# Kernel tuning notes

Hardware: AMD Instinct MI355X
Metric: run time of the kernel (lower is better)

The kernel has to match this reference:

```python
import jax, jax.numpy as jnp
import numpy as np

ITER_STEPS = 2  # matches init_kwargs iteration_steps


def setup_inputs() -> dict:
    key = jax.random.key(0)
    ks = jax.random.split(key, 7)
    B, N, D = 16, 1024, 128
    s = 1.0 / np.sqrt(D).astype(np.float32)
    return {
        "node": jax.random.normal(ks[0], (B, N, D), jnp.float32),
        "node_mask": jax.random.randint(ks[1], (B, N), 0, 2, jnp.int32),
        "graph": jax.random.randint(ks[2], (B, N, N), 0, 2, jnp.int32),
        "w_weight": jax.random.normal(ks[3], (D, 1), jnp.float32) * s,
        "b_weight": jnp.zeros((1,), jnp.float32),
        "w_self": jax.random.normal(ks[4], (D, D), jnp.float32) * s,
        "b_self": jnp.zeros((D,), jnp.float32),
        "w_left": jax.random.normal(ks[5], (D, D), jnp.float32) * s,
        "w_right": jax.random.normal(ks[6], (D, D), jnp.float32) * s,
    }


def reference(node, node_mask, graph, w_weight, b_weight, w_self, b_self, w_left, w_right):
    B, N, D = node.shape
    dt = node.dtype
    nm = node_mask.astype(dt)
    g = graph.astype(dt)  # graph[:, :N, :N] slice is identity here
    diag = jnp.eye(N, dtype=dt)
    # pairwise validity mask, zero diagonal (no self loops)
    pair = nm[:, None, :] * nm[:, :, None] * (1.0 - diag)
    gl = pair * g            # edges present in graph
    gr = pair * (1.0 - g)    # complement edges
    nnum = gl.sum(-1) + gr.sum(-1)
    # replace_masked_values(nnum, nnum>=1, 1): avoid div-by-zero for isolated nodes
    nnum = jnp.where(nnum >= 1.0, nnum, jnp.ones((), dt))
    ws = []
    for _ in range(ITER_STEPS):
        node_weight = jax.nn.sigmoid(node @ w_weight + b_weight)[..., 0]  # [B, N]
        ws.append(node_weight)
        self_info = node @ w_self + b_self
        # replace_masked_values(weight_bcast, mask, 0) == weight * mask (mask is 0/1)
        left = jnp.einsum('bij,bjd->bid', node_weight[:, None, :] * gl, node @ w_left)
        right = jnp.einsum('bij,bjd->bid', node_weight[:, None, :] * gr, node @ w_right)
        node = jax.nn.relu(self_info + (left + right) / nnum[..., None])
    all_node_weight = jnp.stack(ws, axis=1)  # [B, ITER_STEPS, N]
    return node, all_node_weight
```

## Files before the change

kernel.cpp:

```cpp
#include <hip/hip_runtime.h>
#include <math.h>


constexpr int B = 16, N = 1024, D = 128, ITERS = 2;

typedef unsigned short u16;
typedef unsigned char u8;
typedef unsigned int u32;
typedef __attribute__((ext_vector_type(8))) short short8v;
typedef __attribute__((ext_vector_type(4))) unsigned int uint4v;
typedef __attribute__((ext_vector_type(4))) float float4v;

__device__ inline u16 f32_to_bf16(float f) {
  u32 bits = __float_as_uint(f);
  bits += 0x7FFFu + ((bits >> 16) & 1u);
  return (u16)(bits >> 16);
}

__device__ __forceinline__ void map_brt(int blk, int& b, int& rt) {
  int slot = blk >> 3;
  b = ((slot >> 6) << 3) | (blk & 7);
  rt = slot & 63;
}

__global__ __launch_bounds__(256) void wpack_kernel(
    const float* __restrict__ w_self, const float* __restrict__ w_left,
    const float* __restrict__ w_right, const int* __restrict__ mask,
    u16* __restrict__ wsF, u16* __restrict__ wlF, u16* __restrict__ wrF,
    float* __restrict__ sb) {
  int blk = blockIdx.x, tid = threadIdx.x;
  if (blk < 12) {
    int widx = blk >> 2, seg = blk & 3;
    const float* W = (widx == 0) ? w_self : (widx == 1) ? w_left : w_right;
    u16* WF = (widx == 0) ? wsF : (widx == 1) ? wlF : wrF;
#pragma unroll
    for (int q = 0; q < 16; ++q) {
      int o = seg * 4096 + q * 256 + tid;
      int e = o & 7, lane = (o >> 3) & 63, ks = (o >> 9) & 3, cblk = o >> 11;
      int c = cblk * 16 + (lane & 15);
      int k = ks * 32 + ((lane >> 4) & 3) * 8 + e;
      WF[o] = f32_to_bf16(W[k * 128 + c]);
    }
  } else {
    int b = tid >> 4, seg = tid & 15;
    const int* mp = mask + b * N + seg * 64;
    int s = 0;
    for (int q = 0; q < 64; ++q) s += mp[q];
    float fs = (float)s;
    fs += __shfl_xor(fs, 8, 16);
    fs += __shfl_xor(fs, 4, 16);
    fs += __shfl_xor(fs, 2, 16);
    fs += __shfl_xor(fs, 1, 16);
    if (seg == 0) sb[b] = fs;
  }
}

__device__ __forceinline__ void prep_body(
    float (*nlds)[132], float* wmrow, float* invrow, int b, int rt, int tid,
    const int* __restrict__ mask, const float* __restrict__ w_weight,
    const float* __restrict__ b_weight, const float* __restrict__ b_self,
    const u16* __restrict__ wsF, const u16* __restrict__ wlF,
    const u16* __restrict__ wrF, const float* __restrict__ sb,
    float* __restrict__ outw_t, float* __restrict__ nsadj, u16* __restrict__ xF,
    float* __restrict__ part) {
  int r0 = rt * 16;
  if (tid < 128) {
    int r = tid >> 3, jj = tid & 7;
    float acc = 0.f;
#pragma unroll
    for (int q = 0; q < 4; ++q) {
      float4 wv = *(const float4*)(w_weight + jj * 16 + q * 4);
      const float* np = &nlds[r][jj * 16 + q * 4];
      acc += np[0] * wv.x + np[1] * wv.y + np[2] * wv.z + np[3] * wv.w;
    }
    acc += __shfl_xor(acc, 4, 8);
    acc += __shfl_xor(acc, 2, 8);
    acc += __shfl_xor(acc, 1, 8);
    if (jj == 0) {
      float w = 1.f / (1.f + expf(-(acc + b_weight[0])));
      outw_t[b * (ITERS * N) + r0 + r] = w;
      float nm = (float)mask[b * N + r0 + r];
      float nnum = fmaxf(nm * (sb[b] - nm), 1.f);
      wmrow[r] = w * nm;
      invrow[r] = nm / nnum;
    }
  }
  __syncthreads();

  int w = tid >> 6, lane = tid & 63;
  int l15 = lane & 15, lg = lane >> 4;
  int ch = w * 32;

  short8v af[4];
#pragma unroll
  for (int ks = 0; ks < 4; ++ks) {
    float tmp[8];
    *(float4*)&tmp[0] = *(const float4*)&nlds[l15][ks * 32 + lg * 8];
    *(float4*)&tmp[4] = *(const float4*)&nlds[l15][ks * 32 + lg * 8 + 4];
    short8v t;
#pragma unroll
    for (int e = 0; e < 8; ++e) t[e] = (short)f32_to_bf16(tmp[e]);
    af[ks] = t;
  }

  float4v aNR[2], aNL[2], aNS[2];
#define RUN_GEMM(WF, ACC)                                                          \
  {                                                                                \
    _Pragma("unroll") for (int cf = 0; cf < 2; ++cf) {                             \
      ACC[cf] = (float4v){0.f, 0.f, 0.f, 0.f};                                     \
      int cblk = w * 2 + cf;                                                       \
      const u16* bp = (WF) + (((cblk * 4) * 64 + lane) << 3);                      \
      _Pragma("unroll") for (int ks = 0; ks < 4; ++ks) {                           \
        short8v bf = *(const short8v*)(bp + ks * 512);                             \
        ACC[cf] =                                                                  \
            __builtin_amdgcn_mfma_f32_16x16x32_bf16(af[ks], bf, ACC[cf], 0, 0, 0); \
      }                                                                            \
    }                                                                              \
  }
  RUN_GEMM(wrF, aNR);
  RUN_GEMM(wlF, aNL);
  RUN_GEMM(wsF, aNS);
#undef RUN_GEMM

  float wmv[4], invv[4];
#pragma unroll
  for (int j = 0; j < 4; ++j) {
    int rloc = lg * 4 + j;
    wmv[j] = wmrow[rloc];
    invv[j] = invrow[rloc];
  }
  int kch = rt >> 1;
  int lane_f = ((rt & 1) * 2 + (lg >> 1)) * 16;
  int e0 = (lg & 1) * 4;
  float pv[2] = {0.f, 0.f};
#pragma unroll
  for (int cf = 0; cf < 2; ++cf) {
    int col = ch + cf * 16 + l15;
    float bsv = b_self[col];
    u16 xb[4];
#pragma unroll
    for (int j = 0; j < 4; ++j) {
      float x = wmv[j] * (aNL[cf][j] - aNR[cf][j]);
      float v = wmv[j] * aNR[cf][j];
      pv[cf] += v;
      nsadj[((size_t)b * N + r0 + lg * 4 + j) * D + col] =
          aNS[cf][j] + bsv - invv[j] * v;
      xb[j] = f32_to_bf16(x);
    }
    int cblk = w * 2 + cf;
    size_t fi = ((((size_t)b * 8 + cblk) * 32 + kch) * 64 + lane_f + l15) * 8 + e0;
    *(ushort4*)&xF[fi] = *(ushort4*)&xb[0];
  }
#pragma unroll
  for (int cf = 0; cf < 2; ++cf) {
    pv[cf] += __shfl_xor(pv[cf], 16);
    pv[cf] += __shfl_xor(pv[cf], 32);
  }
  if (lg == 0) {
#pragma unroll
    for (int cf = 0; cf < 2; ++cf)
      part[((size_t)b * 64 + rt) * 128 + ch + cf * 16 + l15] = pv[cf];
  }
}

__device__ __forceinline__ void agg_tile(
    const u8* __restrict__ gpk, const u16* __restrict__ xF,
    const float* __restrict__ part, const float* __restrict__ sb,
    const int* __restrict__ mask, const float* __restrict__ nsadj, int b, int r0,
    int tid, float (*accbuf)[16][132], float* vt_s, float ov[8]) {
  if (tid < 128) {
    float s = 0.f;
#pragma unroll
    for (int p = 0; p < 64; ++p) s += part[((size_t)b * 64 + p) * 128 + tid];
    vt_s[tid] = s;
  }
  int w = tid >> 6, lane = tid & 63;
  int l15 = lane & 15, lg = lane >> 4;
  int ks = w;
  const u8* gr = gpk + ((size_t)b * N + r0 + l15) * 128 + lg * 32 + ks * 8;
  uint2 q = *(const uint2*)gr;
  u32 qa[2] = {q.x, q.y};

  const u16* xb = xF + ((((size_t)b * 8) * 32 + ks * 8) * 64 + lane) * 8;

  float4v acc[8] = {{0.f, 0.f, 0.f, 0.f}, {0.f, 0.f, 0.f, 0.f},
                    {0.f, 0.f, 0.f, 0.f}, {0.f, 0.f, 0.f, 0.f},
                    {0.f, 0.f, 0.f, 0.f}, {0.f, 0.f, 0.f, 0.f},
                    {0.f, 0.f, 0.f, 0.f}, {0.f, 0.f, 0.f, 0.f}};
  short8v bcur[8], bnxt[8];
#pragma unroll
  for (int cf = 0; cf < 8; ++cf) bcur[cf] = *(const short8v*)(xb + cf * 16384);
#pragma unroll
  for (int cl = 0; cl < 8; ++cl) {
    if (cl + 1 < 8) {
#pragma unroll
      for (int cf = 0; cf < 8; ++cf)
        bnxt[cf] = *(const short8v*)(xb + cf * 16384 + (cl + 1) * 512);
    }
    u32 by = (qa[cl >> 2] >> ((cl & 3) * 8)) & 255u;
    u32 e0 = ((by & 1u) ? 0x3F80u : 0u) | ((by & 2u) ? 0x3F800000u : 0u);
    u32 e1 = ((by & 4u) ? 0x3F80u : 0u) | ((by & 8u) ? 0x3F800000u : 0u);
    u32 e2 = ((by & 16u) ? 0x3F80u : 0u) | ((by & 32u) ? 0x3F800000u : 0u);
    u32 e3 = ((by & 64u) ? 0x3F80u : 0u) | ((by & 128u) ? 0x3F800000u : 0u);
    uint4v ev = {e0, e1, e2, e3};
    short8v a = __builtin_bit_cast(short8v, ev);
#pragma unroll
    for (int cf = 0; cf < 8; ++cf)
      acc[cf] =
          __builtin_amdgcn_mfma_f32_16x16x32_bf16(a, bcur[cf], acc[cf], 0, 0, 0);
#pragma unroll
    for (int cf = 0; cf < 8; ++cf) bcur[cf] = bnxt[cf];
  }
#pragma unroll
  for (int cf = 0; cf < 8; ++cf)
#pragma unroll
    for (int j = 0; j < 4; ++j) accbuf[w][lg * 4 + j][cf * 16 + l15] = acc[cf][j];
  __syncthreads();

  int row = w * 4 + (lane >> 4);
  int colb = (tid & 15) * 8;
  int orow = r0 + row;
  float nm = (float)mask[b * N + orow];
  float sbv = sb[b];
  float nnum = fmaxf(nm * (sbv - nm), 1.f);
  float inv = nm / nnum;
  const float* nsp = nsadj + ((size_t)b * N + orow) * D + colb;
  float4 n0 = *(const float4*)nsp;
  float4 n1 = *(const float4*)(nsp + 4);
  float nsa[8] = {n0.x, n0.y, n0.z, n0.w, n1.x, n1.y, n1.z, n1.w};
#pragma unroll
  for (int e = 0; e < 8; ++e) {
    int c = colb + e;
    float m = accbuf[0][row][c] + accbuf[1][row][c] + accbuf[2][row][c] +
              accbuf[3][row][c] + vt_s[c];
    ov[e] = fmaxf(nsa[e] + inv * m, 0.f);
  }
}

__global__ __launch_bounds__(256, 4) void pack_prep_kernel(
    const float* __restrict__ node, const int* __restrict__ graph,
    const int* __restrict__ mask, const float* __restrict__ w_weight,
    const float* __restrict__ b_weight, const float* __restrict__ b_self,
    const u16* __restrict__ wsF, const u16* __restrict__ wlF,
    const u16* __restrict__ wrF, const float* __restrict__ sb,
    u8* __restrict__ gpk, float* __restrict__ outw, float* __restrict__ nsadjA,
    u16* __restrict__ xFA, float* __restrict__ partA) {
  __shared__ float nlds[16][132];
  __shared__ float wmrow[16], invrow[16];
  int tid = threadIdx.x;
  int blk = blockIdx.x;

  if (blk < 2048) {
    int gidx = blk * 256 + tid;
#pragma unroll
    for (int it = 0; it < 4; ++it, gidx += 2048 * 256) {
      int j = gidx & 127;
      int rowg = gidx >> 7;
      int i = rowg & (N - 1);
      const int* gp = graph + ((size_t)rowg << 10) + j * 8;
      int4 a = *(const int4*)gp;
      int4 c = *(const int4*)(gp + 4);
      u32 by = (u32)(a.x != 0) | ((u32)(a.y != 0) << 1) | ((u32)(a.z != 0) << 2) |
               ((u32)(a.w != 0) << 3) | ((u32)(c.x != 0) << 4) |
               ((u32)(c.y != 0) << 5) | ((u32)(c.z != 0) << 6) |
               ((u32)(c.w != 0) << 7);
      if (j == (i >> 3)) by &= ~(1u << (i & 7));
      gpk[((size_t)rowg << 7) + (j & 3) * 32 + (j >> 2)] = (u8)by;
    }
    return;
  }

  int pblk = blk - 2048;
  int b, rt;
  map_brt(pblk, b, rt);
  int r0 = rt * 16;

  const float* nbase = node + ((size_t)b * N + r0) * D;
#pragma unroll
  for (int p = 0; p < 2; ++p) {
    int g = p * 256 + tid;
    int row = g >> 5, c4 = g & 31;
    *(float4*)&nlds[row][c4 * 4] = *(const float4*)(nbase + row * 128 + c4 * 4);
  }
  __syncthreads();

  prep_body(nlds, wmrow, invrow, b, rt, tid, mask, w_weight, b_weight, b_self, wsF,
            wlF, wrF, sb, outw, nsadjA, xFA, partA);
}

__global__ __launch_bounds__(256, 3) void agg_prep_kernel(
    const u8* __restrict__ gpk, const int* __restrict__ mask,
    const float* __restrict__ w_weight, const float* __restrict__ b_weight,
    const float* __restrict__ b_self, const u16* __restrict__ wsF,
    const u16* __restrict__ wlF, const u16* __restrict__ wrF,
    const float* __restrict__ sb, const float* __restrict__ nsadjA,
    const u16* __restrict__ xFA, const float* __restrict__ partA,
    float* __restrict__ outw, float* __restrict__ nsadjB, u16* __restrict__ xFB,
    float* __restrict__ partB) {
  __shared__ float accbuf[4][16][132];
  __shared__ float vt_s[128];
  __shared__ float nlds[16][132];
  __shared__ float wmrow[16], invrow[16];
  int tid = threadIdx.x;
  int b, rt;
  map_brt(blockIdx.x, b, rt);
  int r0 = rt * 16;

  float ov[8];
  agg_tile(gpk, xFA, partA, sb, mask, nsadjA, b, r0, tid, accbuf, vt_s, ov);

  int row = (tid >> 6) * 4 + ((tid & 63) >> 4);
  int colb = (tid & 15) * 8;
#pragma unroll
  for (int e = 0; e < 8; ++e) nlds[row][colb + e] = ov[e];
  __syncthreads();

  prep_body(nlds, wmrow, invrow, b, rt, tid, mask, w_weight, b_weight, b_self, wsF,
            wlF, wrF, sb, outw + N , nsadjB, xFB, partB);
}

__global__ __launch_bounds__(256, 4) void agg_fin_kernel(
    const u8* __restrict__ gpk, const int* __restrict__ mask,
    const float* __restrict__ sb, const float* __restrict__ nsadjB,
    const u16* __restrict__ xFB, const float* __restrict__ partB,
    float* __restrict__ out) {
  __shared__ float accbuf[4][16][132];
  __shared__ float vt_s[128];
  int tid = threadIdx.x;
  int b, rt;
  map_brt(blockIdx.x, b, rt);
  int r0 = rt * 16;

  float ov[8];
  agg_tile(gpk, xFB, partB, sb, mask, nsadjB, b, r0, tid, accbuf, vt_s, ov);

  int row = (tid >> 6) * 4 + ((tid & 63) >> 4);
  int colb = (tid & 15) * 8;
  float* op = out + ((size_t)b * N + r0 + row) * D + colb;
  float4 o0 = {ov[0], ov[1], ov[2], ov[3]};
  float4 o1 = {ov[4], ov[5], ov[6], ov[7]};
  *(float4*)op = o0;
  *(float4*)(op + 4) = o1;
}

extern "C" void kernel_launch(void* const* d_in, const int* in_sizes, int n_in,
                              void* d_out, int out_size, void* d_ws, size_t ws_size,
                              hipStream_t stream) {
  const float* node0 = (const float*)d_in[0];
  const int* mask = (const int*)d_in[1];
  const int* graph = (const int*)d_in[2];
  const float* w_weight = (const float*)d_in[3];
  const float* b_weight = (const float*)d_in[4];
  const float* w_self = (const float*)d_in[5];
  const float* b_self = (const float*)d_in[6];
  const float* w_left = (const float*)d_in[7];
  const float* w_right = (const float*)d_in[8];
  float* out = (float*)d_out;
  float* outw = out + (size_t)B * N * D;

  char* ws = (char*)d_ws;
  const size_t MB = 1024 * 1024;
  float* nsadjA = (float*)ws;
  float* nsadjB = (float*)(ws + 8 * MB);
  u16* xFA = (u16*)(ws + 16 * MB);
  u16* xFB = (u16*)(ws + 20 * MB);
  u8* gpk = (u8*)(ws + 24 * MB);
  u16* wsF = (u16*)(ws + 26 * MB);
  u16* wlF = wsF + 16384;
  u16* wrF = wlF + 16384;
  float* partA = (float*)(ws + 26 * MB + 3 * 32768);
  float* partB = partA + (size_t)B * 64 * 128;
  float* sb = partB + (size_t)B * 64 * 128;

  wpack_kernel<<<13, 256, 0, stream>>>(w_self, w_left, w_right, mask, wsF, wlF,
                                       wrF, sb);
  pack_prep_kernel<<<3072, 256, 0, stream>>>(node0, graph, mask, w_weight,
                                             b_weight, b_self, wsF, wlF, wrF, sb,
                                             gpk, outw, nsadjA, xFA, partA);
  agg_prep_kernel<<<1024, 256, 0, stream>>>(gpk, mask, w_weight, b_weight, b_self,
                                            wsF, wlF, wrF, sb, nsadjA, xFA, partA,
                                            outw, nsadjB, xFB, partB);
  agg_fin_kernel<<<1024, 256, 0, stream>>>(gpk, mask, sb, nsadjB, xFB, partB, out);
}
```

Before: 67.44 us.

## Aggregate 32-row tiles with per-wave column split and 512-thread blocks

The aggregation kernels now give each block 32 output rows with 512 threads. Each wave owns a 16-column slice and runs the full K loop over two row sets, so each B fragment is reused for two MFMAs. This removes the cross-wave LDS reduction over K and halves redundant xF reads per row. The part-sum reduction is split across thread groups, and the graph packing loop issues all its loads before processing. The cost is a longer serial MFMA dependency chain per wave and less latency hiding from fewer, larger blocks.

```diff
diff --git a/kernel.cpp b/kernel.cpp
--- a/kernel.cpp
+++ b/kernel.cpp
@@ -15,6 +15,15 @@
   u32 bits = __float_as_uint(f);
   bits += 0x7FFFu + ((bits >> 16) & 1u);
   return (u16)(bits >> 16);
+}
+
+__device__ __forceinline__ short8v expand_byte(u32 by) {
+  u32 e0 = ((by & 1u) ? 0x3F80u : 0u) | ((by & 2u) ? 0x3F800000u : 0u);
+  u32 e1 = ((by & 4u) ? 0x3F80u : 0u) | ((by & 8u) ? 0x3F800000u : 0u);
+  u32 e2 = ((by & 16u) ? 0x3F80u : 0u) | ((by & 32u) ? 0x3F800000u : 0u);
+  u32 e3 = ((by & 64u) ? 0x3F80u : 0u) | ((by & 128u) ? 0x3F800000u : 0u);
+  uint4v ev = {e0, e1, e2, e3};
+  return __builtin_bit_cast(short8v, ev);
 }
 
 __device__ __forceinline__ void map_brt(int blk, int& b, int& rt) {
@@ -163,78 +172,73 @@
   }
 }
 
-__device__ __forceinline__ void agg_tile(
+__device__ __forceinline__ void agg32_core(
     const u8* __restrict__ gpk, const u16* __restrict__ xF,
     const float* __restrict__ part, const float* __restrict__ sb,
     const int* __restrict__ mask, const float* __restrict__ nsadj, int b, int r0,
-    int tid, float (*accbuf)[16][132], float* vt_s, float ov[8]) {
-  if (tid < 128) {
+    int tid, float (*red)[128], float ov[8]) {
+  {
+    int col = tid & 127, grp = tid >> 7;
     float s = 0.f;
 #pragma unroll
-    for (int p = 0; p < 64; ++p) s += part[((size_t)b * 64 + p) * 128 + tid];
-    vt_s[tid] = s;
-  }
-  int w = tid >> 6, lane = tid & 63;
+    for (int p = 0; p < 16; ++p)
+      s += part[((size_t)b * 64 + grp * 16 + p) * 128 + col];
+    red[grp][col] = s;
+  }
+  int wv = tid >> 6, lane = tid & 63;
   int l15 = lane & 15, lg = lane >> 4;
-  int ks = w;
-  const u8* gr = gpk + ((size_t)b * N + r0 + l15) * 128 + lg * 32 + ks * 8;
-  uint2 q = *(const uint2*)gr;
-  u32 qa[2] = {q.x, q.y};
-
-  const u16* xb = xF + ((((size_t)b * 8) * 32 + ks * 8) * 64 + lane) * 8;
-
-  float4v acc[8] = {{0.f, 0.f, 0.f, 0.f}, {0.f, 0.f, 0.f, 0.f},
-                    {0.f, 0.f, 0.f, 0.f}, {0.f, 0.f, 0.f, 0.f},
-                    {0.f, 0.f, 0.f, 0.f}, {0.f, 0.f, 0.f, 0.f},
-                    {0.f, 0.f, 0.f, 0.f}, {0.f, 0.f, 0.f, 0.f}};
-  short8v bcur[8], bnxt[8];
-#pragma unroll
-  for (int cf = 0; cf < 8; ++cf) bcur[cf] = *(const short8v*)(xb + cf * 16384);
-#pragma unroll
-  for (int cl = 0; cl < 8; ++cl) {
-    if (cl + 1 < 8) {
-#pragma unroll
-      for (int cf = 0; cf < 8; ++cf)
-        bnxt[cf] = *(const short8v*)(xb + cf * 16384 + (cl + 1) * 512);
-    }
-    u32 by = (qa[cl >> 2] >> ((cl & 3) * 8)) & 255u;
-    u32 e0 = ((by & 1u) ? 0x3F80u : 0u) | ((by & 2u) ? 0x3F800000u : 0u);
-    u32 e1 = ((by & 4u) ? 0x3F80u : 0u) | ((by & 8u) ? 0x3F800000u : 0u);
-    u32 e2 = ((by & 16u) ? 0x3F80u : 0u) | ((by & 32u) ? 0x3F800000u : 0u);
-    u32 e3 = ((by & 64u) ? 0x3F80u : 0u) | ((by & 128u) ? 0x3F800000u : 0u);
-    uint4v ev = {e0, e1, e2, e3};
-    short8v a = __builtin_bit_cast(short8v, ev);
-#pragma unroll
-    for (int cf = 0; cf < 8; ++cf)
-      acc[cf] =
-          __builtin_amdgcn_mfma_f32_16x16x32_bf16(a, bcur[cf], acc[cf], 0, 0, 0);
-#pragma unroll
-    for (int cf = 0; cf < 8; ++cf) bcur[cf] = bnxt[cf];
-  }
-#pragma unroll
-  for (int cf = 0; cf < 8; ++cf)
-#pragma unroll
-    for (int j = 0; j < 4; ++j) accbuf[w][lg * 4 + j][cf * 16 + l15] = acc[cf][j];
+
+  const u8* g0 = gpk + ((size_t)b * N + r0 + l15) * 128 + lg * 32;
+  uint4 qA = *(const uint4*)g0;
+  uint4 qB = *(const uint4*)(g0 + 16);
+  uint4 qC = *(const uint4*)(g0 + 16 * 128);
+  uint4 qD = *(const uint4*)(g0 + 16 * 128 + 16);
+  u32 q0[8] = {qA.x, qA.y, qA.z, qA.w, qB.x, qB.y, qB.z, qB.w};
+  u32 q1[8] = {qC.x, qC.y, qC.z, qC.w, qD.x, qD.y, qD.z, qD.w};
+
+  const u16* xb = xF + (((size_t)b * 8 + wv) * 32) * 512 + lane * 8;
+
+  float4v acc0 = {0.f, 0.f, 0.f, 0.f};
+  float4v acc1 = {0.f, 0.f, 0.f, 0.f};
+  short8v b0 = *(const short8v*)(xb);
+  short8v b1 = *(const short8v*)(xb + 512);
+#pragma unroll
+  for (int cl = 0; cl < 32; ++cl) {
+    short8v b2 = b0;
+    if (cl + 2 < 32) b2 = *(const short8v*)(xb + (cl + 2) * 512);
+    u32 by0 = (q0[cl >> 2] >> ((cl & 3) * 8)) & 255u;
+    u32 by1 = (q1[cl >> 2] >> ((cl & 3) * 8)) & 255u;
+    short8v a0 = expand_byte(by0);
+    short8v a1 = expand_byte(by1);
+    acc0 = __builtin_amdgcn_mfma_f32_16x16x32_bf16(a0, b0, acc0, 0, 0, 0);
+    acc1 = __builtin_amdgcn_mfma_f32_16x16x32_bf16(a1, b0, acc1, 0, 0, 0);
+    b0 = b1;
+    b1 = b2;
+  }
   __syncthreads();
 
-  int row = w * 4 + (lane >> 4);
-  int colb = (tid & 15) * 8;
-  int orow = r0 + row;
-  float nm = (float)mask[b * N + orow];
   float sbv = sb[b];
-  float nnum = fmaxf(nm * (sbv - nm), 1.f);
-  float inv = nm / nnum;
-  const float* nsp = nsadj + ((size_t)b * N + orow) * D + colb;
-  float4 n0 = *(const float4*)nsp;
-  float4 n1 = *(const float4*)(nsp + 4);
-  float nsa[8] = {n0.x, n0.y, n0.z, n0.w, n1.x, n1.y, n1.z, n1.w};
-#pragma unroll
-  for (int e = 0; e < 8; ++e) {
-    int c = colb + e;
-    float m = accbuf[0][row][c] + accbuf[1][row][c] + accbuf[2][row][c] +
-              accbuf[3][row][c] + vt_s[c];
-    ov[e] = fmaxf(nsa[e] + inv * m, 0.f);
-  }
+  int col = wv * 16 + l15;
+  float vt = red[0][col] + red[1][col] + red[2][col] + red[3][col];
+#pragma unroll
+  for (int rs = 0; rs < 2; ++rs) {
+#pragma unroll
+    for (int j = 0; j < 4; ++j) {
+      float a = (rs == 0) ? acc0[j] : acc1[j];
+      int orow = r0 + rs * 16 + lg * 4 + j;
+      float nm = (float)mask[b * N + orow];
+      float nnum = fmaxf(nm * (sbv - nm), 1.f);
+      float inv = nm / nnum;
+      size_t off = ((size_t)b * N + orow) * D + col;
+      ov[rs * 4 + j] = fmaxf(nsadj[off] + inv * (a + vt), 0.f);
+    }
+  }
+}
+
+__device__ __forceinline__ void map_brt32(int blk, int& b, int& rt32) {
+  int slot = blk >> 3;
+  b = ((slot >> 5) << 3) | (blk & 7);
+  rt32 = slot & 31;
 }
 
 __global__ __launch_bounds__(256, 4) void pack_prep_kernel(
@@ -251,15 +255,22 @@
   int blk = blockIdx.x;
 
   if (blk < 2048) {
-    int gidx = blk * 256 + tid;
-#pragma unroll
-    for (int it = 0; it < 4; ++it, gidx += 2048 * 256) {
-      int j = gidx & 127;
-      int rowg = gidx >> 7;
+    int gidx0 = blk * 256 + tid;
+    int4 ra[4][2];
+#pragma unroll
+    for (int it = 0; it < 4; ++it) {
+      int gidx = gidx0 + it * (2048 * 256);
+      int j = gidx & 127, rowg = gidx >> 7;
+      const int* gp = graph + ((size_t)rowg << 10) + j * 8;
+      ra[it][0] = *(const int4*)gp;
+      ra[it][1] = *(const int4*)(gp + 4);
+    }
+#pragma unroll
+    for (int it = 0; it < 4; ++it) {
+      int gidx = gidx0 + it * (2048 * 256);
+      int j = gidx & 127, rowg = gidx >> 7;
       int i = rowg & (N - 1);
-      const int* gp = graph + ((size_t)rowg << 10) + j * 8;
-      int4 a = *(const int4*)gp;
-      int4 c = *(const int4*)(gp + 4);
+      int4 a = ra[it][0], c = ra[it][1];
       u32 by = (u32)(a.x != 0) | ((u32)(a.y != 0) << 1) | ((u32)(a.z != 0) << 2) |
                ((u32)(a.w != 0) << 3) | ((u32)(c.x != 0) << 4) |
                ((u32)(c.y != 0) << 5) | ((u32)(c.z != 0) << 6) |
@@ -288,7 +299,7 @@
             wlF, wrF, sb, outw, nsadjA, xFA, partA);
 }
 
-__global__ __launch_bounds__(256, 3) void agg_prep_kernel(
+__global__ __launch_bounds__(512, 4) void agg_prep_kernel(
     const u8* __restrict__ gpk, const int* __restrict__ mask,
     const float* __restrict__ w_weight, const float* __restrict__ b_weight,
     const float* __restrict__ b_self, const u16* __restrict__ wsF,
@@ -297,50 +308,57 @@
     const u16* __restrict__ xFA, const float* __restrict__ partA,
     float* __restrict__ outw, float* __restrict__ nsadjB, u16* __restrict__ xFB,
     float* __restrict__ partB) {
-  __shared__ float accbuf[4][16][132];
-  __shared__ float vt_s[128];
-  __shared__ float nlds[16][132];
-  __shared__ float wmrow[16], invrow[16];
+  __shared__ float red[4][128];
+  __shared__ float nlds[32][132];
+  __shared__ float wmrow[32], invrow[32];
   int tid = threadIdx.x;
-  int b, rt;
-  map_brt(blockIdx.x, b, rt);
-  int r0 = rt * 16;
+  int b, rt32;
+  map_brt32(blockIdx.x, b, rt32);
+  int r0 = rt32 * 32;
 
   float ov[8];
-  agg_tile(gpk, xFA, partA, sb, mask, nsadjA, b, r0, tid, accbuf, vt_s, ov);
-
-  int row = (tid >> 6) * 4 + ((tid & 63) >> 4);
-  int colb = (tid & 15) * 8;
-#pragma unroll
-  for (int e = 0; e < 8; ++e) nlds[row][colb + e] = ov[e];
+  agg32_core(gpk, xFA, partA, sb, mask, nsadjA, b, r0, tid, red, ov);
+
+  int wv = tid >> 6, lane = tid & 63;
+  int l15 = lane & 15, lg = lane >> 4;
+  int col = wv * 16 + l15;
+#pragma unroll
+  for (int rs = 0; rs < 2; ++rs)
+#pragma unroll
+    for (int j = 0; j < 4; ++j) nlds[rs * 16 + lg * 4 + j][col] = ov[rs * 4 + j];
   __syncthreads();
 
-  prep_body(nlds, wmrow, invrow, b, rt, tid, mask, w_weight, b_weight, b_self, wsF,
-            wlF, wrF, sb, outw + N , nsadjB, xFB, partB);
-}
-
-__global__ __launch_bounds__(256, 4) void agg_fin_kernel(
+  int half = tid >> 8;
+  int tid2 = tid & 255;
+  prep_body((float(*)[132]) & nlds[half * 16][0], &wmrow[half * 16],
+            &invrow[half * 16], b, rt32 * 2 + half, tid2, mask, w_weight,
+            b_weight, b_self, wsF, wlF, wrF, sb, outw + N, nsadjB, xFB, partB);
+}
+
+__global__ __launch_bounds__(512, 4) void agg_fin_kernel(
     const u8* __restrict__ gpk, const int* __restrict__ mask,
     const float* __restrict__ sb, const float* __restrict__ nsadjB,
     const u16* __restrict__ xFB, const float* __restrict__ partB,
     float* __restrict__ out) {
-  __shared__ float accbuf[4][16][132];
-  __shared__ float vt_s[128];
+  __shared__ float red[4][128];
   int tid = threadIdx.x;
-  int b, rt;
-  map_brt(blockIdx.x, b, rt);
-  int r0 = rt * 16;
+  int b, rt32;
+  map_brt32(blockIdx.x, b, rt32);
+  int r0 = rt32 * 32;
 
   float ov[8];
-  agg_tile(gpk, xFB, partB, sb, mask, nsadjB, b, r0, tid, accbuf, vt_s, ov);
-
-  int row = (tid >> 6) * 4 + ((tid & 63) >> 4);
-  int colb = (tid & 15) * 8;
-  float* op = out + ((size_t)b * N + r0 + row) * D + colb;
-  float4 o0 = {ov[0], ov[1], ov[2], ov[3]};
-  float4 o1 = {ov[4], ov[5], ov[6], ov[7]};
-  *(float4*)op = o0;
-  *(float4*)(op + 4) = o1;
+  agg32_core(gpk, xFB, partB, sb, mask, nsadjB, b, r0, tid, red, ov);
+
+  int wv = tid >> 6, lane = tid & 63;
+  int l15 = lane & 15, lg = lane >> 4;
+  int col = wv * 16 + l15;
+#pragma unroll
+  for (int rs = 0; rs < 2; ++rs)
+#pragma unroll
+    for (int j = 0; j < 4; ++j) {
+      int orow = r0 + rs * 16 + lg * 4 + j;
+      out[((size_t)b * N + orow) * D + col] = ov[rs * 4 + j];
+    }
 }
 
 extern "C" void kernel_launch(void* const* d_in, const int* in_sizes, int n_in,
@@ -377,8 +395,8 @@
   pack_prep_kernel<<<3072, 256, 0, stream>>>(node0, graph, mask, w_weight,
                                              b_weight, b_self, wsF, wlF, wrF, sb,
                                              gpk, outw, nsadjA, xFA, partA);
-  agg_prep_kernel<<<1024, 256, 0, stream>>>(gpk, mask, w_weight, b_weight, b_self,
-                                            wsF, wlF, wrF, sb, nsadjA, xFA, partA,
-                                            outw, nsadjB, xFB, partB);
-  agg_fin_kernel<<<1024, 256, 0, stream>>>(gpk, mask, sb, nsadjB, xFB, partB, out);
-}
+  agg_prep_kernel<<<512, 512, 0, stream>>>(gpk, mask, w_weight, b_weight, b_self,
+                                           wsF, wlF, wrF, sb, nsadjA, xFA, partA,
+                                           outw, nsadjB, xFB, partB);
+  agg_fin_kernel<<<512, 512, 0, stream>>>(gpk, mask, sb, nsadjB, xFB, partB, out);
+}
```

Measured after the change: 60.66 us (median of 2 runs). -10.1%, faster.
